# Kernel tuning notes

Measured on AMD Instinct MI355X. Metric: run time of the kernel, lower is better.

The kernel has to match this reference:

```python
import jax, jax.numpy as jnp
import numpy as np

D_MODEL = 768
NUM_HEADS = 12
HEAD_DIM = D_MODEL // NUM_HEADS
THETA = 10000.0
SEQ = 4096
BATCH = 2


def setup_inputs() -> dict:
    key = jax.random.key(0)
    ks = jax.random.split(key, 5)
    std = np.sqrt(2.0 / (D_MODEL + D_MODEL)).astype(np.float32)
    x = jax.random.normal(ks[0], (BATCH, SEQ, D_MODEL), dtype=jnp.float32)
    token_positions = jnp.arange(SEQ, dtype=jnp.int32)
    # Linear stores weight as (d_out, d_in), applied as x @ W.T
    wq = jax.random.normal(ks[1], (D_MODEL, D_MODEL), dtype=jnp.float32) * std
    wk = jax.random.normal(ks[2], (D_MODEL, D_MODEL), dtype=jnp.float32) * std
    wv = jax.random.normal(ks[3], (D_MODEL, D_MODEL), dtype=jnp.float32) * std
    wo = jax.random.normal(ks[4], (D_MODEL, D_MODEL), dtype=jnp.float32) * std
    return {"x": x, "token_positions": token_positions,
            "wq": wq, "wk": wk, "wv": wv, "wo": wo}


def _apply_rope(t, positions):
    # t: [B, H, S, hd], positions: [S]
    half = HEAD_DIM // 2
    inv_freq = THETA ** (-jnp.arange(0, HEAD_DIM, 2, dtype=jnp.float32) / HEAD_DIM)  # [half]
    angles = positions.astype(jnp.float32)[:, None] * inv_freq  # [S, half]
    cos = jnp.repeat(jnp.cos(angles), 2, axis=-1)  # [S, hd]
    sin = jnp.repeat(jnp.sin(angles), 2, axis=-1)  # [S, hd]
    # rotate pairs: (-x1, x0, -x3, x2, ...)
    t2 = jnp.stack([-t[..., 1::2], t[..., ::2]], axis=-1).reshape(t.shape)
    return t * cos + t2 * sin


def reference(x, token_positions, wq, wk, wv, wo):
    B, S, D = x.shape
    H, hd = NUM_HEADS, HEAD_DIM
    q = (x @ wq.T).reshape(B, S, H, hd).transpose(0, 2, 1, 3)  # [B,H,S,hd]
    k = (x @ wk.T).reshape(B, S, H, hd).transpose(0, 2, 1, 3)
    v = (x @ wv.T).reshape(B, S, H, hd).transpose(0, 2, 1, 3)
    q = _apply_rope(q, token_positions)
    k = _apply_rope(k, token_positions)
    scale = hd ** -0.5
    scores = jnp.einsum('bhqd,bhkd->bhqk', q, k) * scale  # [B,H,S,S]
    causal = jnp.tril(jnp.ones((S, S), dtype=bool))
    scores = jnp.where(causal, scores, -jnp.inf)
    att = jax.nn.softmax(scores, axis=-1)
    out = jnp.einsum('bhqk,bhkd->bhqd', att, v)  # [B,H,S,hd]
    out = out.transpose(0, 2, 1, 3).reshape(B, S, D)
    return out @ wo.T
```

## Files before the change

### kernel.cpp

```cpp
#include <hip/hip_runtime.h>
#include <hip/hip_bf16.h>
#include <stdint.h>

#define D_MODEL 768
#define NHEADS 12
#define HD 64
#define SEQ 4096
#define BATCH 2
#define MTOT (BATCH*SEQ)
#define BHN (BATCH*NHEADS)

typedef __attribute__((ext_vector_type(8))) short short8;
typedef __attribute__((ext_vector_type(4))) float f32x4;
typedef __attribute__((ext_vector_type(16))) float f32x16;
typedef __attribute__((ext_vector_type(4))) int i32x4;

__device__ inline unsigned short f2bf(float f) {
  union { float f; unsigned u; } v; v.f = f;
  unsigned r = (v.u + 0x7FFFu + ((v.u >> 16) & 1u)) >> 16;
  return (unsigned short)r;
}
__device__ inline unsigned cvtpk_bf16(float lo, float hi) {
  unsigned r;
  asm("v_cvt_pk_bf16_f32 %0, %1, %2" : "=v"(r) : "v"(lo), "v"(hi));
  return r;
}
__device__ inline void perm32swap(unsigned &a, unsigned &b) {
  asm("v_permlane32_swap_b32 %0, %1" : "+v"(a), "+v"(b));
}
__device__ inline float exp2fast(float x) {
  float r;
  asm("v_exp_f32 %0, %1" : "=v"(r) : "v"(x));
  return r;
}
__device__ inline void gload16(const void* g, void* l) {
  __builtin_amdgcn_global_load_lds(
      (const __attribute__((address_space(1))) unsigned int*)g,
      (__attribute__((address_space(3))) unsigned int*)l, 16, 0, 0);
}

__global__ void k_conv(const float* __restrict__ x,  const float* __restrict__ wq,
                       const float* __restrict__ wk, const float* __restrict__ wv,
                       const float* __restrict__ wo,
                       unsigned short* __restrict__ xb,  unsigned short* __restrict__ wqb,
                       unsigned short* __restrict__ wkb, unsigned short* __restrict__ wvb,
                       unsigned short* __restrict__ wob)
{
  int i = blockIdx.x * blockDim.x + threadIdx.x;
  const int X4 = MTOT*D_MODEL/4;
  const int W4 = D_MODEL*D_MODEL/4;
  const float* src; unsigned short* dst; int idx;
  if (i < X4) { src = x; dst = xb; idx = i; }
  else {
    int j = i - X4;
    if      (j <   W4) { src = wq; dst = wqb; idx = j; }
    else if (j < 2*W4) { src = wk; dst = wkb; idx = j -   W4; }
    else if (j < 3*W4) { src = wv; dst = wvb; idx = j - 2*W4; }
    else if (j < 4*W4) { src = wo; dst = wob; idx = j - 3*W4; }
    else return;
  }
  float4 v = ((const float4*)src)[idx];
  ushort4 o;
  o.x = f2bf(v.x); o.y = f2bf(v.y); o.z = f2bf(v.z); o.w = f2bf(v.w);
  ((ushort4*)dst)[idx] = o;
}

__global__ void k_ropetab(const int* __restrict__ pos, float* __restrict__ ct, float* __restrict__ st) {
  int i = blockIdx.x * blockDim.x + threadIdx.x;
  if (i >= SEQ*32) return;
  int s = i & (SEQ-1), j = i >> 12;
  float p = (float)pos[s];
  const float L = 0.2878231366242557f;
  float freq = __expf(-L * (float)j);
  float a = p * freq;
  ct[i] = cosf(a);
  st[i] = sinf(a);
}

__global__ __launch_bounds__(256)
void k_gemm_qkv(const unsigned short* __restrict__ X,
                const unsigned short* __restrict__ Wq,
                const unsigned short* __restrict__ Wk,
                const unsigned short* __restrict__ Wv,
                unsigned short* __restrict__ Qp,
                unsigned short* __restrict__ Kp,
                unsigned short* __restrict__ VT,
                const float* __restrict__ ct,
                const float* __restrict__ st)
{
  __shared__ __align__(16) unsigned short As[2][128*32];
  __shared__ __align__(16) unsigned short Bs[2][128*32];
  const int tid = threadIdx.x;
  const int wave = tid >> 6, lane = tid & 63;
  const int lr = lane & 15, lg = lane >> 4;
  const int wr = wave >> 1, wc = wave & 1;
  const int m0 = blockIdx.x * 128;
  const int n0 = blockIdx.y * 128;
  const int z  = blockIdx.z;
  const unsigned short* B = (z == 0) ? Wq : (z == 1) ? Wk : Wv;
  const int K = 768;

  f32x4 acc[4][4] = {};
  const int srow = tid >> 2, scol = (tid & 3) << 3;
  const unsigned short* ag = X + (size_t)(m0 + srow) * K + scol;
  const unsigned short* bg = B + (size_t)(n0 + srow) * K + scol;

  {
    char* a0 = (char*)As[0] + wave*1024;
    char* a1 = (char*)As[0] + 4096 + wave*1024;
    char* b0 = (char*)Bs[0] + wave*1024;
    char* b1 = (char*)Bs[0] + 4096 + wave*1024;
    gload16(ag, a0);
    gload16(ag + (size_t)64*K, a1);
    gload16(bg, b0);
    gload16(bg + (size_t)64*K, b1);
  }
  int cur = 0;
  for (int k0 = 0; k0 < K; k0 += 32) {
    __syncthreads();
    if (k0 + 32 < K) {
      char* a0 = (char*)As[cur^1] + wave*1024;
      char* a1 = (char*)As[cur^1] + 4096 + wave*1024;
      char* b0 = (char*)Bs[cur^1] + wave*1024;
      char* b1 = (char*)Bs[cur^1] + 4096 + wave*1024;
      gload16(ag + k0 + 32, a0);
      gload16(ag + (size_t)64*K + k0 + 32, a1);
      gload16(bg + k0 + 32, b0);
      gload16(bg + (size_t)64*K + k0 + 32, b1);
    }
    short8 af[4], bfr[4];
    #pragma unroll
    for (int i = 0; i < 4; ++i)
      af[i] = *(const short8*)&As[cur][(wr*64 + i*16 + lr)*32 + lg*8];
    #pragma unroll
    for (int j = 0; j < 4; ++j)
      bfr[j] = *(const short8*)&Bs[cur][(wc*64 + j*16 + lr)*32 + lg*8];
    #pragma unroll
    for (int i = 0; i < 4; ++i)
      #pragma unroll
      for (int j = 0; j < 4; ++j)
        acc[i][j] = __builtin_amdgcn_mfma_f32_16x16x32_bf16(af[i], bfr[j], acc[i][j], 0, 0, 0);
    cur ^= 1;
  }

  #pragma unroll
  for (int i = 0; i < 4; ++i)
    #pragma unroll
    for (int j = 0; j < 4; ++j) {
      const int n = n0 + wc*64 + j*16 + lr;
      const int h = n >> 6, d = n & (HD-1);
      if (z == 2) {
        #pragma unroll
        for (int r = 0; r < 4; ++r) {
          int m = m0 + wr*64 + i*16 + lg*4 + r;
          int bb = m >> 12, s = m & (SEQ-1);
          VT[(((size_t)bb*NHEADS + h)*HD + d)*SEQ + s] = f2bf(acc[i][j][r]);
        }
      } else {
        unsigned short* dst = (z == 0) ? Qp : Kp;
        const int jrow = d >> 1;
        const int mb = m0 + wr*64 + i*16 + lg*4;
        const int bb = mb >> 12;
        const int sbase = mb & (SEQ-1);
        f32x4 cs4 = *(const f32x4*)(ct + (size_t)jrow*SEQ + sbase);
        f32x4 sn4 = *(const f32x4*)(st + (size_t)jrow*SEQ + sbase);
        #pragma unroll
        for (int r = 0; r < 4; ++r) {
          float vv = acc[i][j][r];
          float pp = __shfl_xor(vv, 1);
          float res = (d & 1) ? (vv*cs4[r] + pp*sn4[r]) : (vv*cs4[r] - pp*sn4[r]);
          if (z == 0) res *= 0.18033688011112043f;
          dst[(((size_t)bb*NHEADS + h)*SEQ + (sbase + r))*HD + d] = f2bf(res);
        }
      }
    }
}

__global__ __launch_bounds__(256)
void k_gemm_wo(const unsigned short* __restrict__ X,
               const unsigned short* __restrict__ W,
               float* __restrict__ out)
{
  __shared__ __align__(16) unsigned short As[2][128*32];
  __shared__ __align__(16) unsigned short Bs[2][128*32];
  const int tid = threadIdx.x;
  const int wave = tid >> 6, lane = tid & 63;
  const int lr = lane & 15, lg = lane >> 4;
  const int wr = wave >> 1, wc = wave & 1;
  const int m0 = blockIdx.x * 128;
  const int n0 = blockIdx.y * 128;
  const int K = 768;

  f32x4 acc[4][4] = {};
  const int srow = tid >> 2, scol = (tid & 3) << 3;
  const unsigned short* ag = X + (size_t)(m0 + srow) * K + scol;
  const unsigned short* bg = W + (size_t)(n0 + srow) * K + scol;

  {
    char* a0 = (char*)As[0] + wave*1024;
    char* a1 = (char*)As[0] + 4096 + wave*1024;
    char* b0 = (char*)Bs[0] + wave*1024;
    char* b1 = (char*)Bs[0] + 4096 + wave*1024;
    gload16(ag, a0);
    gload16(ag + (size_t)64*K, a1);
    gload16(bg, b0);
    gload16(bg + (size_t)64*K, b1);
  }
  int cur = 0;
  for (int k0 = 0; k0 < K; k0 += 32) {
    __syncthreads();
    if (k0 + 32 < K) {
      char* a0 = (char*)As[cur^1] + wave*1024;
      char* a1 = (char*)As[cur^1] + 4096 + wave*1024;
      char* b0 = (char*)Bs[cur^1] + wave*1024;
      char* b1 = (char*)Bs[cur^1] + 4096 + wave*1024;
      gload16(ag + k0 + 32, a0);
      gload16(ag + (size_t)64*K + k0 + 32, a1);
      gload16(bg + k0 + 32, b0);
      gload16(bg + (size_t)64*K + k0 + 32, b1);
    }
    short8 af[4], bfr[4];
    #pragma unroll
    for (int i = 0; i < 4; ++i)
      af[i] = *(const short8*)&As[cur][(wr*64 + i*16 + lr)*32 + lg*8];
    #pragma unroll
    for (int j = 0; j < 4; ++j)
      bfr[j] = *(const short8*)&Bs[cur][(wc*64 + j*16 + lr)*32 + lg*8];
    #pragma unroll
    for (int i = 0; i < 4; ++i)
      #pragma unroll
      for (int j = 0; j < 4; ++j)
        acc[i][j] = __builtin_amdgcn_mfma_f32_16x16x32_bf16(af[i], bfr[j], acc[i][j], 0, 0, 0);
    cur ^= 1;
  }

  #pragma unroll
  for (int i = 0; i < 4; ++i)
    #pragma unroll
    for (int j = 0; j < 4; ++j)
      #pragma unroll
      for (int r = 0; r < 4; ++r) {
        int m = m0 + wr*64 + i*16 + lg*4 + r;
        int n = n0 + wc*64 + j*16 + lr;
        out[(size_t)m*D_MODEL + n] = acc[i][j][r];
      }
}

__global__ __launch_bounds__(128, 3)
void k_attn(const unsigned short* __restrict__ Qp,
            const unsigned short* __restrict__ Kp,
            const unsigned short* __restrict__ VT,
            unsigned short* __restrict__ AO)
{
  __shared__ __align__(16) unsigned short Ks[2][64*64];
  __shared__ __align__(16) unsigned short Vs[2][64*64];

  const int tid = threadIdx.x;
  const int wave = tid >> 6, lane = tid & 63;
  const int qcol = lane & 31, hi = lane >> 5;

  const int u = blockIdx.x;
  const int kk = u >> 8, g = u & 255;
  const int rank = (kk & 1) ? ((kk + 1) * 256 - 1 - g) : (kk * 256 + g);
  const int chunk = 63 - rank / 24;
  const int bh = rank % 24;

  const int b = bh / NHEADS, h = bh % NHEADS;
  const int qw = chunk * 64 + wave * 32;
  const int nt = chunk + 1;

  const unsigned short* Qh = Qp + (size_t)bh * SEQ * HD;
  const unsigned short* Kh = Kp + (size_t)bh * SEQ * HD;
  const unsigned short* Vh = VT + (size_t)bh * HD * SEQ;

  short8 qf[4];
  #pragma unroll
  for (int ds = 0; ds < 4; ++ds)
    qf[ds] = *(const short8*)(Qh + (size_t)(qw + qcol)*HD + ds*16 + hi*8);

  short8 onesf;
  #pragma unroll
  for (int i = 0; i < 8; ++i) onesf[i] = (short)0x3F80;

  f32x16 o[2] = {};
  f32x16 lacc = {};

  const int g_row = tid >> 3;
  const int sgp = ((tid & 7) ^ (g_row & 7)) * 8;

  auto STAGE = [&](int t, int bi) {
    const size_t kb = (size_t)t * 64;
    #pragma unroll
    for (int bp = 0; bp < 4; ++bp) {
      const int row = bp*16 + g_row;
      gload16(Kh + (kb + row)*HD + sgp,            (char*)Ks[bi] + bp*2048 + wave*1024);
      gload16(Vh + (size_t)row*SEQ + kb + sgp,     (char*)Vs[bi] + bp*2048 + wave*1024);
    }
  };

  STAGE(0, 0);
  __syncthreads();

  int cur = 0;
  for (int kt = 0; kt < nt; ++kt) {
    if (kt + 1 < nt) STAGE(kt + 1, cur ^ 1);
    const char* Kb = (const char*)Ks[cur];
    const char* Vb = (const char*)Vs[cur];
    f32x16 c[2];
    __builtin_amdgcn_s_setprio(1);
    #pragma unroll
    for (int kc = 0; kc < 2; ++kc) {
      f32x16 acc = {};
      #pragma unroll
      for (int ds = 0; ds < 4; ++ds) {
        const int row = kc*32 + qcol;
        short8 kf = *(const short8*)(Kb + row*128 + ((ds*32 + hi*16) ^ ((row & 7) << 4)));
        acc = __builtin_amdgcn_mfma_f32_32x32x16_bf16(kf, qf[ds], acc, 0, 0, 0);
      }
      c[kc] = acc;
    }
    __builtin_amdgcn_s_setprio(0);
    if (kt == nt - 1) {
      const int q = qw + qcol;
      #pragma unroll
      for (int kc = 0; kc < 2; ++kc)
        #pragma unroll
        for (int r = 0; r < 16; ++r) {
          int key = kt*64 + kc*32 + (r & 3) + 8*(r >> 2) + 4*hi;
          if (key > q) c[kc][r] = -1e30f;
        }
    }
    #pragma unroll
    for (int kc = 0; kc < 2; ++kc)
      #pragma unroll
      for (int r = 0; r < 16; ++r)
        c[kc][r] = exp2fast(c[kc][r]);
    unsigned U[8][2];
    #pragma unroll
    for (int g2 = 0; g2 < 8; ++g2) {
      const int fc = g2 >> 2, gq = g2 & 3;
      U[g2][0] = cvtpk_bf16(c[fc][4*gq + 0], c[fc][4*gq + 1]);
      U[g2][1] = cvtpk_bf16(c[fc][4*gq + 2], c[fc][4*gq + 3]);
    }
    #pragma unroll
    for (int ks = 0; ks < 4; ++ks) {
      unsigned j0 = U[2*ks][0], j2 = U[2*ks+1][0];
      perm32swap(j0, j2);
      unsigned j1 = U[2*ks][1], j3 = U[2*ks+1][1];
      perm32swap(j1, j3);
      union { unsigned u[4]; short8 s; } pf;
      pf.u[0] = j0; pf.u[1] = j1; pf.u[2] = j2; pf.u[3] = j3;
      __builtin_amdgcn_s_setprio(1);
      #pragma unroll
      for (int dc = 0; dc < 2; ++dc) {
        const int row = dc*32 + qcol;
        short8 vf = *(const short8*)(Vb + row*128 + ((ks*32 + hi*16) ^ ((row & 7) << 4)));
        o[dc] = __builtin_amdgcn_mfma_f32_32x32x16_bf16(vf, pf.s, o[dc], 0, 0, 0);
      }
      lacc = __builtin_amdgcn_mfma_f32_32x32x16_bf16(onesf, pf.s, lacc, 0, 0, 0);
      __builtin_amdgcn_s_setprio(0);
    }
    __syncthreads();
    cur ^= 1;
  }

  const float inv = 1.0f / lacc[0];
  const size_t rowbase = ((size_t)b*SEQ + qw + qcol) * D_MODEL + h*HD;
  #pragma unroll
  for (int dc = 0; dc < 2; ++dc)
    #pragma unroll
    for (int g2 = 0; g2 < 4; ++g2) {
      ushort4 pk;
      pk.x = f2bf(o[dc][4*g2 + 0] * inv);
      pk.y = f2bf(o[dc][4*g2 + 1] * inv);
      pk.z = f2bf(o[dc][4*g2 + 2] * inv);
      pk.w = f2bf(o[dc][4*g2 + 3] * inv);
      const int d0 = dc*32 + 8*g2 + 4*hi;
      *(ushort4*)(AO + rowbase + d0) = pk;
    }
}

extern "C" void kernel_launch(void* const* d_in, const int* in_sizes, int n_in,
                              void* d_out, int out_size, void* d_ws, size_t ws_size,
                              hipStream_t stream)
{
  const float* x  = (const float*)d_in[0];
  const int* posi = (const int*)d_in[1];
  const float* wq = (const float*)d_in[2];
  const float* wk = (const float*)d_in[3];
  const float* wv = (const float*)d_in[4];
  const float* wo = (const float*)d_in[5];
  float* out = (float*)d_out;

  char* ws = (char*)d_ws;
  size_t off = 0;
  auto alloc = [&](size_t bytes) {
    char* p = ws + off;
    off += (bytes + 255) & ~(size_t)255;
    return p;
  };
  unsigned short* xb  = (unsigned short*)alloc((size_t)MTOT*D_MODEL*2);
  unsigned short* wqb = (unsigned short*)alloc((size_t)D_MODEL*D_MODEL*2);
  unsigned short* wkb = (unsigned short*)alloc((size_t)D_MODEL*D_MODEL*2);
  unsigned short* wvb = (unsigned short*)alloc((size_t)D_MODEL*D_MODEL*2);
  unsigned short* wob = (unsigned short*)alloc((size_t)D_MODEL*D_MODEL*2);
  unsigned short* Qb  = (unsigned short*)alloc((size_t)BHN*SEQ*HD*2);
  unsigned short* Kb  = (unsigned short*)alloc((size_t)BHN*SEQ*HD*2);
  unsigned short* VTb = (unsigned short*)alloc((size_t)BHN*HD*SEQ*2);
  unsigned short* AOb = (unsigned short*)alloc((size_t)MTOT*D_MODEL*2);
  float* ct = (float*)alloc((size_t)SEQ*32*4);
  float* st = (float*)alloc((size_t)SEQ*32*4);

  const int total4 = MTOT*D_MODEL/4 + 4*(D_MODEL*D_MODEL/4);
  k_conv<<<(total4 + 255)/256, 256, 0, stream>>>(x, wq, wk, wv, wo, xb, wqb, wkb, wvb, wob);
  k_ropetab<<<(SEQ*32 + 255)/256, 256, 0, stream>>>(posi, ct, st);

  k_gemm_qkv<<<dim3(MTOT/128, D_MODEL/128, 3), 256, 0, stream>>>(xb, wqb, wkb, wvb, Qb, Kb, VTb, ct, st);
  k_attn<<<dim3(1536), 128, 0, stream>>>(Qb, Kb, VTb, AOb);
  k_gemm_wo<<<dim3(MTOT/128, D_MODEL/128), 256, 0, stream>>>(AOb, wob, out);
}
```

Measured before the change: 167.4 us.

## Load K and V fragments directly from global memory, dropping LDS staging

The attention kernel no longer stages K and V tiles through double-buffered shared memory with async loads and block barriers. Each wave now reads its MFMA operand fragments straight from global memory into registers every key tile. This removes the LDS traffic and the per-tile __syncthreads, but both waves in a block now fetch the same K/V data separately. It also loses the prefetch overlap, so global latency is exposed unless the compiler hoists the loads.

```diff
diff --git a/kernel.cpp b/kernel.cpp
--- a/kernel.cpp
+++ b/kernel.cpp
@@ -252,9 +252,6 @@
             const unsigned short* __restrict__ VT,
             unsigned short* __restrict__ AO)
 {
-  __shared__ __align__(16) unsigned short Ks[2][64*64];
-  __shared__ __align__(16) unsigned short Vs[2][64*64];
-
   const int tid = threadIdx.x;
   const int wave = tid >> 6, lane = tid & 63;
   const int qcol = lane & 31, hi = lane >> 5;
@@ -285,41 +282,42 @@
   f32x16 o[2] = {};
   f32x16 lacc = {};
 
-  const int g_row = tid >> 3;
-  const int sgp = ((tid & 7) ^ (g_row & 7)) * 8;
-
-  auto STAGE = [&](int t, int bi) {
-    const size_t kb = (size_t)t * 64;
-    #pragma unroll
-    for (int bp = 0; bp < 4; ++bp) {
-      const int row = bp*16 + g_row;
-      gload16(Kh + (kb + row)*HD + sgp,            (char*)Ks[bi] + bp*2048 + wave*1024);
-      gload16(Vh + (size_t)row*SEQ + kb + sgp,     (char*)Vs[bi] + bp*2048 + wave*1024);
-    }
-  };
-
-  STAGE(0, 0);
-  __syncthreads();
-
-  int cur = 0;
+  const unsigned short* k0p = Kh + (size_t)qcol*HD + hi*8;
+  const unsigned short* k1p = Kh + (size_t)(32 + qcol)*HD + hi*8;
+  const unsigned short* v0p = Vh + (size_t)qcol*SEQ + hi*8;
+  const unsigned short* v1p = Vh + (size_t)(32 + qcol)*SEQ + hi*8;
+
   for (int kt = 0; kt < nt; ++kt) {
-    if (kt + 1 < nt) STAGE(kt + 1, cur ^ 1);
-    const char* Kb = (const char*)Ks[cur];
-    const char* Vb = (const char*)Vs[cur];
+    const size_t kb = (size_t)kt * 64;
+    short8 kf0[4], kf1[4];
+    #pragma unroll
+    for (int ds = 0; ds < 4; ++ds) {
+      kf0[ds] = *(const short8*)(k0p + kb*HD + ds*16);
+      kf1[ds] = *(const short8*)(k1p + kb*HD + ds*16);
+    }
     f32x16 c[2];
     __builtin_amdgcn_s_setprio(1);
-    #pragma unroll
-    for (int kc = 0; kc < 2; ++kc) {
-      f32x16 acc = {};
-      #pragma unroll
-      for (int ds = 0; ds < 4; ++ds) {
-        const int row = kc*32 + qcol;
-        short8 kf = *(const short8*)(Kb + row*128 + ((ds*32 + hi*16) ^ ((row & 7) << 4)));
-        acc = __builtin_amdgcn_mfma_f32_32x32x16_bf16(kf, qf[ds], acc, 0, 0, 0);
-      }
-      c[kc] = acc;
+    {
+      f32x16 a = {};
+      #pragma unroll
+      for (int ds = 0; ds < 4; ++ds)
+        a = __builtin_amdgcn_mfma_f32_32x32x16_bf16(kf0[ds], qf[ds], a, 0, 0, 0);
+      c[0] = a;
+    }
+    {
+      f32x16 a = {};
+      #pragma unroll
+      for (int ds = 0; ds < 4; ++ds)
+        a = __builtin_amdgcn_mfma_f32_32x32x16_bf16(kf1[ds], qf[ds], a, 0, 0, 0);
+      c[1] = a;
     }
     __builtin_amdgcn_s_setprio(0);
+    short8 vf[4][2];
+    #pragma unroll
+    for (int ks = 0; ks < 4; ++ks) {
+      vf[ks][0] = *(const short8*)(v0p + kb + ks*16);
+      vf[ks][1] = *(const short8*)(v1p + kb + ks*16);
+    }
     if (kt == nt - 1) {
       const int q = qw + qcol;
       #pragma unroll
@@ -351,17 +349,11 @@
       union { unsigned u[4]; short8 s; } pf;
       pf.u[0] = j0; pf.u[1] = j1; pf.u[2] = j2; pf.u[3] = j3;
       __builtin_amdgcn_s_setprio(1);
-      #pragma unroll
-      for (int dc = 0; dc < 2; ++dc) {
-        const int row = dc*32 + qcol;
-        short8 vf = *(const short8*)(Vb + row*128 + ((ks*32 + hi*16) ^ ((row & 7) << 4)));
-        o[dc] = __builtin_amdgcn_mfma_f32_32x32x16_bf16(vf, pf.s, o[dc], 0, 0, 0);
-      }
-      lacc = __builtin_amdgcn_mfma_f32_32x32x16_bf16(onesf, pf.s, lacc, 0, 0, 0);
+      o[0] = __builtin_amdgcn_mfma_f32_32x32x16_bf16(vf[ks][0], pf.s, o[0], 0, 0, 0);
+      o[1] = __builtin_amdgcn_mfma_f32_32x32x16_bf16(vf[ks][1], pf.s, o[1], 0, 0, 0);
+      lacc  = __builtin_amdgcn_mfma_f32_32x32x16_bf16(onesf, pf.s, lacc, 0, 0, 0);
       __builtin_amdgcn_s_setprio(0);
     }
-    __syncthreads();
-    cur ^= 1;
   }
 
   const float inv = 1.0f / lacc[0];
```

Result: slower. 262.6 us (+56.8%).
